# Performance work log

Measured on AMD Instinct MI355X. Metric: run time of the kernel, lower is better.

## Reference

```python
import jax, jax.numpy as jnp
import numpy as np

N_NODES = 100000
N_EDGES = 1600000
NFEAT = 128
NHID = 128


def setup_inputs() -> dict:
    key = jax.random.key(0)
    k1, k2, k3, k4 = jax.random.split(key, 4)
    x = jax.random.normal(k1, (N_NODES, NFEAT), dtype=jnp.float32)
    edge_index = jax.random.randint(k2, (2, N_EDGES), 0, N_NODES, dtype=jnp.int64)
    # GCNConv params (glorot-style scale)
    W1 = jax.random.normal(k3, (NFEAT, NHID), dtype=jnp.float32) * (1.0 / np.sqrt(NFEAT))
    b1 = jnp.zeros((NHID,), dtype=jnp.float32)
    return {"x": x, "edge_index": edge_index, "W1": W1, "b1": b1}


def gcn_conv(x, edge_index, W, b):
    # PyG GCNConv: out = D^{-1/2} (A + I) D^{-1/2} (x W) + b
    n = x.shape[0]
    loop = jnp.arange(n, dtype=edge_index.dtype)
    src = jnp.concatenate([edge_index[0], loop])  # message sources
    dst = jnp.concatenate([edge_index[1], loop])  # aggregation targets
    deg = jax.ops.segment_sum(jnp.ones_like(dst, dtype=x.dtype), dst, num_segments=n)
    dinv = jnp.where(deg > 0, jax.lax.rsqrt(deg), 0.0)
    norm = dinv[src] * dinv[dst]  # [E+N]
    h = x @ W  # [N, nhid]
    msg = h[src] * norm[:, None]  # gather + scale, [E+N, nhid]
    out = jax.ops.segment_sum(msg, dst, num_segments=n) + b
    return out


def reference(x, edge_index, W1, b1):
    # forward = gc1(x, edge_index) followed by dropout (identity in eval mode)
    return gcn_conv(x, edge_index, W1, b1)
```

## Files before the change

### kernel.cpp

```cpp
#include <hip/hip_runtime.h>
#include <math.h>


#define N_NODES 100000
#define N_EDGES 1600000
#define NF 128
#define LDW 136

#define BSHIFT 9
#define NBUCK 196
#define CHUNK 4096
#define NCHUNK 392
#define GEMM_BLOCKS 1563

typedef short bf16x8 __attribute__((ext_vector_type(8)));
typedef float f32x4  __attribute__((ext_vector_type(4)));
typedef unsigned short u16;

__device__ inline u16 f2bf(float f) {
    unsigned int u = __float_as_uint(f);
    return (u16)((u + 0x7fffu + ((u >> 16) & 1u)) >> 16);
}

__device__ inline f32x4 unpack4(unsigned int u) {
    f32x4 r;
    r[0] = (float)(signed char)(u & 0xff);
    r[1] = (float)(signed char)((u >> 8) & 0xff);
    r[2] = (float)(signed char)((u >> 16) & 0xff);
    r[3] = (float)(signed char)(u >> 24);
    return r;
}

__global__ __launch_bounds__(256) void fused1_kernel(const float* __restrict__ x,
                                                     const float* __restrict__ W,
                                                     signed char* __restrict__ h8,
                                                     float* __restrict__ rscale,
                                                     const int* __restrict__ ei,
                                                     int* __restrict__ histG,
                                                     int* __restrict__ bsum) {
    __shared__ u16 Wt[NF * LDW];
    __shared__ u16 xs[64 * LDW];
    const int t = threadIdx.x;

    if (blockIdx.x >= GEMM_BLOCKS) {
        int* hl = (int*)Wt;
        const int c = blockIdx.x - GEMM_BLOCKS;
        for (int b = t; b < NBUCK; b += 256) hl[b] = 0;
        __syncthreads();
        const int e0 = c * CHUNK;
        #pragma unroll 4
        for (int it = 0; it < CHUNK / 256; ++it) {
            int e = e0 + it * 256 + t;
            if (e < N_EDGES) atomicAdd(&hl[ei[N_EDGES + e] >> BSHIFT], 1);
        }
        __syncthreads();
        for (int b = t; b < NBUCK; b += 256) {
            int v = hl[b];
            histG[b * NCHUNK + c] = v;
            if (v) atomicAdd(&bsum[b], v);
        }
        return;
    }

    const int lane = t & 63;
    const int w = t >> 6;
    const int quad = lane >> 4;
    const int m = lane & 15;

    for (int idx = t; idx < NF * NF; idx += 256) {
        int k = idx >> 7, n = idx & 127;
        Wt[n * LDW + k] = f2bf(W[idx]);
    }

    const int rowbase = blockIdx.x * 64;
    for (int it = 0; it < 8; ++it) {
        int linear = it * 256 + t;
        int row = linear >> 5, colq = linear & 31;
        int grow = rowbase + row;
        float4 v = (grow < N_NODES) ? ((const float4*)x)[grow * 32 + colq]
                                    : make_float4(0.f, 0.f, 0.f, 0.f);
        u16* p = &xs[row * LDW + colq * 4];
        p[0] = f2bf(v.x); p[1] = f2bf(v.y); p[2] = f2bf(v.z); p[3] = f2bf(v.w);
    }
    __syncthreads();

    f32x4 acc[8];
    #pragma unroll
    for (int nt = 0; nt < 8; ++nt) acc[nt] = (f32x4){0.f, 0.f, 0.f, 0.f};

    const int r0 = w * 16;
    #pragma unroll
    for (int kt = 0; kt < 4; ++kt) {
        const int k0 = kt * 32;
        bf16x8 a = *(const bf16x8*)&xs[(r0 + m) * LDW + k0 + quad * 8];
        #pragma unroll
        for (int nt = 0; nt < 8; ++nt) {
            bf16x8 bb = *(const bf16x8*)&Wt[(nt * 16 + m) * LDW + k0 + quad * 8];
            acc[nt] = __builtin_amdgcn_mfma_f32_16x16x32_bf16(a, bb, acc[nt], 0, 0, 0);
        }
    }

    float rmax[4];
    #pragma unroll
    for (int r = 0; r < 4; ++r) {
        float mx = 0.f;
        #pragma unroll
        for (int nt = 0; nt < 8; ++nt) mx = fmaxf(mx, fabsf(acc[nt][r]));
        #pragma unroll
        for (int off = 1; off < 16; off <<= 1) mx = fmaxf(mx, __shfl_xor(mx, off));
        rmax[r] = fmaxf(mx, 1e-20f);
    }

    __syncthreads();
    char* xs8 = (char*)xs;
    #pragma unroll
    for (int r = 0; r < 4; ++r) {
        const float inv = 127.f / rmax[r];
        const int row = r0 + quad * 4 + r;
        #pragma unroll
        for (int nt = 0; nt < 8; ++nt) {
            int q = __float2int_rn(acc[nt][r] * inv);
            xs8[row * 144 + nt * 16 + m] = (char)q;
        }
        if (m == 0) {
            int grow = rowbase + row;
            if (grow < N_NODES) rscale[grow] = rmax[r] * (1.f / 127.f);
        }
    }
    __syncthreads();

    for (int it = 0; it < 2; ++it) {
        int linear = it * 256 + t;
        int row = linear >> 3, seg = linear & 7;
        int grow = rowbase + row;
        if (grow < N_NODES) {
            uint4 v = *(const uint4*)&xs8[row * 144 + seg * 16];
            ((uint4*)h8)[grow * 8 + seg] = v;
        }
    }
}

__global__ __launch_bounds__(256) void scanS2_kernel(const int* __restrict__ bsum,
                                                     int* __restrict__ bbase) {
    __shared__ int sb[256];
    const int t = threadIdx.x;
    int v = (t < NBUCK) ? bsum[t] : 0;
    sb[t] = v;
    __syncthreads();
    #pragma unroll
    for (int off = 1; off < 256; off <<= 1) {
        int cur = sb[t];
        int add = (t >= off) ? sb[t - off] : 0;
        __syncthreads();
        sb[t] = cur + add;
        __syncthreads();
    }
    if (t < NBUCK) bbase[t] = sb[t] - v;
    if (t == 0) bbase[NBUCK] = N_EDGES;
}

__global__ __launch_bounds__(256) void scanS3_kernel(int* __restrict__ histG,
                                                     const int* __restrict__ bbase) {
    __shared__ int lpair[256];
    const int t = threadIdx.x, b = blockIdx.x;
    int v0 = 0, v1 = 0;
    if (t < NCHUNK / 2) {
        v0 = histG[b * NCHUNK + 2 * t];
        v1 = histG[b * NCHUNK + 2 * t + 1];
    }
    int ps = v0 + v1;
    lpair[t] = ps;
    __syncthreads();
    #pragma unroll
    for (int off = 1; off < 256; off <<= 1) {
        int cur = lpair[t];
        int add = (t >= off) ? lpair[t - off] : 0;
        __syncthreads();
        lpair[t] = cur + add;
        __syncthreads();
    }
    if (t < NCHUNK / 2) {
        int base = bbase[b] + lpair[t] - ps;
        histG[b * NCHUNK + 2 * t] = base;
        histG[b * NCHUNK + 2 * t + 1] = base + v0;
    }
}

__global__ __launch_bounds__(256) void binB_kernel(const int* __restrict__ ei,
                                                   const int* __restrict__ histG,
                                                   unsigned int* __restrict__ ebuf) {
    __shared__ int lbase[NBUCK];
    __shared__ int lcur[NBUCK];
    const int t = threadIdx.x, c = blockIdx.x;
    for (int b = t; b < NBUCK; b += 256) { lbase[b] = histG[b * NCHUNK + c]; lcur[b] = 0; }
    __syncthreads();
    const int e0 = c * CHUNK;
    #pragma unroll 4
    for (int it = 0; it < CHUNK / 256; ++it) {
        int e = e0 + it * 256 + t;
        if (e < N_EDGES) {
            int s = ei[e];
            int d = ei[N_EDGES + e];
            int b = d >> BSHIFT;
            int r = atomicAdd(&lcur[b], 1);
            ebuf[lbase[b] + r] = ((unsigned)(d & 511) << 17) | (unsigned)s;
        }
    }
}

__global__ __launch_bounds__(256) void fill3_kernel(const unsigned int* __restrict__ ebuf,
                                                    const int* __restrict__ bbase,
                                                    const float* __restrict__ rscale,
                                                    int* __restrict__ rowptr,
                                                    float* __restrict__ dinv,
                                                    float* __restrict__ combo,
                                                    int* __restrict__ slot) {
    __shared__ int lcnt[1 << BSHIFT];
    __shared__ int lpair[256];
    __shared__ int lcur[1 << BSHIFT];
    const int t = threadIdx.x, b = blockIdx.x;
    const int n0 = b << BSHIFT;
    lcnt[t] = 0; lcnt[t + 256] = 0;
    __syncthreads();
    const int lo = bbase[b], hi = bbase[b + 1];
    for (int e = lo + t; e < hi; e += 256) {
        atomicAdd(&lcnt[ebuf[e] >> 17], 1);
    }
    __syncthreads();
    int c0 = lcnt[2 * t], c1 = lcnt[2 * t + 1];
    int ps = c0 + c1;
    lpair[t] = ps;
    __syncthreads();
    #pragma unroll
    for (int off = 1; off < 256; off <<= 1) {
        int v = lpair[t];
        int add = (t >= off) ? lpair[t - off] : 0;
        __syncthreads();
        lpair[t] = v + add;
        __syncthreads();
    }
    const int base = lo + lpair[t] - ps;
    lcur[2 * t] = base;
    lcur[2 * t + 1] = base + c0;
    const int n = n0 + 2 * t;
    if (n < N_NODES) {
        float dv = rsqrtf((float)c0 + 1.0f);
        rowptr[n] = base; dinv[n] = dv; combo[n] = dv * rscale[n];
    }
    if (n + 1 < N_NODES) {
        float dv = rsqrtf((float)c1 + 1.0f);
        rowptr[n + 1] = base + c0; dinv[n + 1] = dv; combo[n + 1] = dv * rscale[n + 1];
    }
    if (b == 0 && t == 0) rowptr[N_NODES] = N_EDGES;
    __syncthreads();
    for (int e = lo + t; e < hi; e += 256) {
        unsigned int p = ebuf[e];
        int pos = atomicAdd(&lcur[p >> 17], 1);
        slot[pos] = (int)(p & 0x1ffff);
    }
}

__global__ __launch_bounds__(256) void agg_kernel(const signed char* __restrict__ h8,
                                                  const float* __restrict__ dinv,
                                                  const float* __restrict__ combo,
                                                  const int* __restrict__ rowptr,
                                                  const int* __restrict__ slot,
                                                  const float* __restrict__ b,
                                                  float* __restrict__ out) {
    const int wave = threadIdx.x >> 6;
    const int lane = threadIdx.x & 63;
    const int i = blockIdx.x * 4 + wave;
    if (i >= N_NODES) return;

    const float di = dinv[i];
    const int start = rowptr[i];
    const int m = rowptr[i + 1] - start;
    const int half = lane >> 5;
    const int col = lane & 31;

    const unsigned int* h4 = (const unsigned int*)h8;
    f32x4 acc0 = {0.f, 0.f, 0.f, 0.f};
    f32x4 acc1 = {0.f, 0.f, 0.f, 0.f};

    for (int base = 0; base < m; base += 64) {
        const int mm = min(m - base, 64);
        int   s_l  = (lane < mm) ? slot[start + base + lane] : 0;
        float cw_l = (lane < mm) ? combo[s_l] : 0.0f;
        const int mu = (mm + 7) & ~7;
        for (int j = 0; j < mu; j += 8) {
            #pragma unroll
            for (int q = 0; q < 8; q += 2) {
                int   sj = __shfl(s_l, j + q + half);
                float wj = __shfl(cw_l, j + q + half) * di;
                unsigned int u = h4[sj * 32 + col];
                f32x4 hv = unpack4(u);
                if (q & 2) acc1 += hv * wj;
                else       acc0 += hv * wj;
            }
        }
    }

    f32x4 acc = acc0 + acc1;
    #pragma unroll
    for (int c = 0; c < 4; ++c) acc[c] += __shfl_xor(acc[c], 32);

    if (lane < 32) {
        float4 bb = ((const float4*)b)[col];
        unsigned int uv = h4[i * 32 + col];
        f32x4 hv = unpack4(uv);
        const float w0 = di * combo[i];
        float4 o;
        o.x = bb.x + acc[0] + w0 * hv[0];
        o.y = bb.y + acc[1] + w0 * hv[1];
        o.z = bb.z + acc[2] + w0 * hv[2];
        o.w = bb.w + acc[3] + w0 * hv[3];
        ((float4*)out)[i * 32 + col] = o;
    }
}

extern "C" void kernel_launch(void* const* d_in, const int* in_sizes, int n_in,
                              void* d_out, int out_size, void* d_ws, size_t ws_size,
                              hipStream_t stream) {
    const float* x  = (const float*)d_in[0];
    const int*   ei = (const int*)d_in[1];
    const float* W  = (const float*)d_in[2];
    const float* b  = (const float*)d_in[3];
    float* out = (float*)d_out;

    signed char* h8 = (signed char*)d_ws;
    float* rscale = (float*)d_ws + 3300000;
    float* dinv   = (float*)d_ws + 3400000;
    float* combo  = (float*)d_ws + 3500000;
    int*   rowptr = (int*)d_ws + 3600000;
    int*   bbase  = (int*)d_ws + 3750000;
    int*   bsum   = (int*)d_ws + 3760000;
    int*   histG  = (int*)d_ws + 3770000;
    int*   slot   = (int*)d_ws + 4000000;
    unsigned int* ebuf = (unsigned int*)d_ws + 5700000;

    hipMemsetAsync(bsum, 0, NBUCK * sizeof(int), stream);
    fused1_kernel<<<GEMM_BLOCKS + NCHUNK, 256, 0, stream>>>(x, W, h8, rscale,
                                                            ei, histG, bsum);
    scanS2_kernel<<<1, 256, 0, stream>>>(bsum, bbase);
    scanS3_kernel<<<NBUCK, 256, 0, stream>>>(histG, bbase);
    binB_kernel<<<NCHUNK, 256, 0, stream>>>(ei, histG, ebuf);
    fill3_kernel<<<NBUCK, 256, 0, stream>>>(ebuf, bbase, rscale, rowptr, dinv,
                                            combo, slot);
    agg_kernel<<<N_NODES / 4, 256, 0, stream>>>(h8, dinv, combo, rowptr, slot, b, out);
}
```

Before: 223.5 us.

## Precompute bf16 W image, fuse scans, widen aggregation loads with offset-int8 unpack

A small prep kernel converts W to a padded bf16 transposed image once and zeroes the bucket sums, so each of the GEMM blocks copies the image into shared memory with vector loads instead of converting W itself. The two scan kernels merge into one, with every block redoing the small bucket-sum scan. The aggregation kernel now has each lane load 8 bytes and handle 16 edges per step, using unsigned int8 with a +128 offset that is removed through an accumulated weight-sum correction. The aim is to cut redundant per-block W conversion, one launch and a memset, and per-gather instruction overhead, at the cost of extra shuffles and redundant scan work.

```diff
diff --git a/kernel.cpp b/kernel.cpp
--- a/kernel.cpp
+++ b/kernel.cpp
@@ -22,24 +22,35 @@
     return (u16)((u + 0x7fffu + ((u >> 16) & 1u)) >> 16);
 }
 
-__device__ inline f32x4 unpack4(unsigned int u) {
+__device__ inline f32x4 unpk4u(unsigned int u) {
     f32x4 r;
-    r[0] = (float)(signed char)(u & 0xff);
-    r[1] = (float)(signed char)((u >> 8) & 0xff);
-    r[2] = (float)(signed char)((u >> 16) & 0xff);
-    r[3] = (float)(signed char)(u >> 24);
+    r[0] = (float)(u & 0xffu);
+    r[1] = (float)((u >> 8) & 0xffu);
+    r[2] = (float)((u >> 16) & 0xffu);
+    r[3] = (float)((u >> 24) & 0xffu);
     return r;
 }
 
+__global__ __launch_bounds__(256) void prep_kernel(const float* __restrict__ W,
+                                                   u16* __restrict__ Wimg,
+                                                   int* __restrict__ bsum) {
+    const int t = threadIdx.x;
+    if (blockIdx.x == 0 && t < NBUCK) bsum[t] = 0;
+    for (int idx = blockIdx.x * 256 + t; idx < NF * NF; idx += 16 * 256) {
+        int k = idx >> 7, n = idx & 127;
+        Wimg[n * LDW + k] = f2bf(W[idx]);
+    }
+}
+
 __global__ __launch_bounds__(256) void fused1_kernel(const float* __restrict__ x,
-                                                     const float* __restrict__ W,
+                                                     const u16* __restrict__ Wimg,
                                                      signed char* __restrict__ h8,
                                                      float* __restrict__ rscale,
                                                      const int* __restrict__ ei,
                                                      int* __restrict__ histG,
                                                      int* __restrict__ bsum) {
-    __shared__ u16 Wt[NF * LDW];
-    __shared__ u16 xs[64 * LDW];
+    __shared__ __align__(16) u16 Wt[NF * LDW];
+    __shared__ __align__(16) u16 xs[64 * LDW];
     const int t = threadIdx.x;
 
     if (blockIdx.x >= GEMM_BLOCKS) {
@@ -67,10 +78,8 @@
     const int quad = lane >> 4;
     const int m = lane & 15;
 
-    for (int idx = t; idx < NF * NF; idx += 256) {
-        int k = idx >> 7, n = idx & 127;
-        Wt[n * LDW + k] = f2bf(W[idx]);
-    }
+    for (int idx = t; idx < (NF * LDW * 2) / 16; idx += 256)
+        ((uint4*)Wt)[idx] = ((const uint4*)Wimg)[idx];
 
     const int rowbase = blockIdx.x * 64;
     for (int it = 0; it < 8; ++it) {
@@ -79,8 +88,9 @@
         int grow = rowbase + row;
         float4 v = (grow < N_NODES) ? ((const float4*)x)[grow * 32 + colq]
                                     : make_float4(0.f, 0.f, 0.f, 0.f);
-        u16* p = &xs[row * LDW + colq * 4];
-        p[0] = f2bf(v.x); p[1] = f2bf(v.y); p[2] = f2bf(v.z); p[3] = f2bf(v.w);
+        unsigned a0 = (unsigned)f2bf(v.x) | ((unsigned)f2bf(v.y) << 16);
+        unsigned a1 = (unsigned)f2bf(v.z) | ((unsigned)f2bf(v.w) << 16);
+        *(uint2*)&xs[row * LDW + colq * 4] = make_uint2(a0, a1);
     }
     __syncthreads();
 
@@ -119,7 +129,7 @@
         const int row = r0 + quad * 4 + r;
         #pragma unroll
         for (int nt = 0; nt < 8; ++nt) {
-            int q = __float2int_rn(acc[nt][r] * inv);
+            int q = __float2int_rn(acc[nt][r] * inv) + 128;
             xs8[row * 144 + nt * 16 + m] = (char)q;
         }
         if (m == 0) {
@@ -140,12 +150,15 @@
     }
 }
 
-__global__ __launch_bounds__(256) void scanS2_kernel(const int* __restrict__ bsum,
+__global__ __launch_bounds__(256) void scanS3_kernel(int* __restrict__ histG,
+                                                     const int* __restrict__ bsum,
                                                      int* __restrict__ bbase) {
     __shared__ int sb[256];
-    const int t = threadIdx.x;
-    int v = (t < NBUCK) ? bsum[t] : 0;
-    sb[t] = v;
+    __shared__ int lpair[256];
+    const int t = threadIdx.x, b = blockIdx.x;
+
+    int sv = (t < NBUCK) ? bsum[t] : 0;
+    sb[t] = sv;
     __syncthreads();
     #pragma unroll
     for (int off = 1; off < 256; off <<= 1) {
@@ -155,14 +168,10 @@
         sb[t] = cur + add;
         __syncthreads();
     }
-    if (t < NBUCK) bbase[t] = sb[t] - v;
-    if (t == 0) bbase[NBUCK] = N_EDGES;
-}
-
-__global__ __launch_bounds__(256) void scanS3_kernel(int* __restrict__ histG,
-                                                     const int* __restrict__ bbase) {
-    __shared__ int lpair[256];
-    const int t = threadIdx.x, b = blockIdx.x;
+    const int bb = (b > 0) ? sb[b - 1] : 0;
+    if (t == 0) bbase[b] = bb;
+    if (b == 0 && t == 0) bbase[NBUCK] = N_EDGES;
+
     int v0 = 0, v1 = 0;
     if (t < NCHUNK / 2) {
         v0 = histG[b * NCHUNK + 2 * t];
@@ -180,7 +189,7 @@
         __syncthreads();
     }
     if (t < NCHUNK / 2) {
-        int base = bbase[b] + lpair[t] - ps;
+        int base = bb + lpair[t] - ps;
         histG[b * NCHUNK + 2 * t] = base;
         histG[b * NCHUNK + 2 * t + 1] = base + v0;
     }
@@ -275,46 +284,65 @@
     const float di = dinv[i];
     const int start = rowptr[i];
     const int m = rowptr[i + 1] - start;
-    const int half = lane >> 5;
-    const int col = lane & 31;
-
-    const unsigned int* h4 = (const unsigned int*)h8;
-    f32x4 acc0 = {0.f, 0.f, 0.f, 0.f};
-    f32x4 acc1 = {0.f, 0.f, 0.f, 0.f};
+    const int quad = lane >> 4;
+    const int qcol = lane & 15;
+
+    const uint2* h16 = (const uint2*)h8;
+    f32x4 a0lo = {0.f, 0.f, 0.f, 0.f}, a0hi = {0.f, 0.f, 0.f, 0.f};
+    f32x4 a1lo = {0.f, 0.f, 0.f, 0.f}, a1hi = {0.f, 0.f, 0.f, 0.f};
+    float ws = 0.f;
 
     for (int base = 0; base < m; base += 64) {
         const int mm = min(m - base, 64);
         int   s_l  = (lane < mm) ? slot[start + base + lane] : 0;
         float cw_l = (lane < mm) ? combo[s_l] : 0.0f;
-        const int mu = (mm + 7) & ~7;
-        for (int j = 0; j < mu; j += 8) {
+        const int mu = (mm + 15) & ~15;
+        for (int j = 0; j < mu; j += 16) {
             #pragma unroll
-            for (int q = 0; q < 8; q += 2) {
-                int   sj = __shfl(s_l, j + q + half);
-                float wj = __shfl(cw_l, j + q + half) * di;
-                unsigned int u = h4[sj * 32 + col];
-                f32x4 hv = unpack4(u);
-                if (q & 2) acc1 += hv * wj;
-                else       acc0 += hv * wj;
+            for (int q = 0; q < 16; q += 4) {
+                int   sj = __shfl(s_l,  j + q + quad);
+                float wj = __shfl(cw_l, j + q + quad);
+                uint2 u  = h16[sj * 16 + qcol];
+                ws += wj;
+                f32x4 lo = unpk4u(u.x);
+                f32x4 hi = unpk4u(u.y);
+                if (q & 4) { a1lo += lo * wj; a1hi += hi * wj; }
+                else       { a0lo += lo * wj; a0hi += hi * wj; }
             }
         }
     }
 
-    f32x4 acc = acc0 + acc1;
-    #pragma unroll
-    for (int c = 0; c < 4; ++c) acc[c] += __shfl_xor(acc[c], 32);
-
-    if (lane < 32) {
-        float4 bb = ((const float4*)b)[col];
-        unsigned int uv = h4[i * 32 + col];
-        f32x4 hv = unpack4(uv);
-        const float w0 = di * combo[i];
-        float4 o;
-        o.x = bb.x + acc[0] + w0 * hv[0];
-        o.y = bb.y + acc[1] + w0 * hv[1];
-        o.z = bb.z + acc[2] + w0 * hv[2];
-        o.w = bb.w + acc[3] + w0 * hv[3];
-        ((float4*)out)[i * 32 + col] = o;
+    #pragma unroll
+    for (int c = 0; c < 4; ++c) { a0lo[c] += a1lo[c]; a0hi[c] += a1hi[c]; }
+    #pragma unroll
+    for (int c = 0; c < 4; ++c) {
+        a0lo[c] += __shfl_xor(a0lo[c], 16);
+        a0hi[c] += __shfl_xor(a0hi[c], 16);
+        a0lo[c] += __shfl_xor(a0lo[c], 32);
+        a0hi[c] += __shfl_xor(a0hi[c], 32);
+    }
+    ws += __shfl_xor(ws, 16);
+    ws += __shfl_xor(ws, 32);
+
+    if (lane < 16) {
+        const float ci = combo[i];
+        uint2 us = h16[i * 16 + lane];
+        f32x4 slo = unpk4u(us.x);
+        f32x4 shi = unpk4u(us.y);
+        const float corr = 128.f * (ws + ci);
+        float4 bb0 = ((const float4*)b)[lane * 2];
+        float4 bb1 = ((const float4*)b)[lane * 2 + 1];
+        float4 o0, o1;
+        o0.x = bb0.x + di * (a0lo[0] + ci * slo[0] - corr);
+        o0.y = bb0.y + di * (a0lo[1] + ci * slo[1] - corr);
+        o0.z = bb0.z + di * (a0lo[2] + ci * slo[2] - corr);
+        o0.w = bb0.w + di * (a0lo[3] + ci * slo[3] - corr);
+        o1.x = bb1.x + di * (a0hi[0] + ci * shi[0] - corr);
+        o1.y = bb1.y + di * (a0hi[1] + ci * shi[1] - corr);
+        o1.z = bb1.z + di * (a0hi[2] + ci * shi[2] - corr);
+        o1.w = bb1.w + di * (a0hi[3] + ci * shi[3] - corr);
+        ((float4*)out)[i * 32 + lane * 2] = o0;
+        ((float4*)out)[i * 32 + lane * 2 + 1] = o1;
     }
 }
 
@@ -335,14 +363,14 @@
     int*   bbase  = (int*)d_ws + 3750000;
     int*   bsum   = (int*)d_ws + 3760000;
     int*   histG  = (int*)d_ws + 3770000;
+    u16*   Wimg   = (u16*)((int*)d_ws + 3900000);
     int*   slot   = (int*)d_ws + 4000000;
     unsigned int* ebuf = (unsigned int*)d_ws + 5700000;
 
-    hipMemsetAsync(bsum, 0, NBUCK * sizeof(int), stream);
-    fused1_kernel<<<GEMM_BLOCKS + NCHUNK, 256, 0, stream>>>(x, W, h8, rscale,
+    prep_kernel<<<16, 256, 0, stream>>>(W, Wimg, bsum);
+    fused1_kernel<<<GEMM_BLOCKS + NCHUNK, 256, 0, stream>>>(x, Wimg, h8, rscale,
                                                             ei, histG, bsum);
-    scanS2_kernel<<<1, 256, 0, stream>>>(bsum, bbase);
-    scanS3_kernel<<<NBUCK, 256, 0, stream>>>(histG, bbase);
+    scanS3_kernel<<<NBUCK, 256, 0, stream>>>(histG, bsum, bbase);
     binB_kernel<<<NCHUNK, 256, 0, stream>>>(ei, histG, ebuf);
     fill3_kernel<<<NBUCK, 256, 0, stream>>>(ebuf, bbase, rscale, rowptr, dinv,
                                             combo, slot);
```

New measurement: 224.0 us. About the same (+0.2%).
